# Kernel optimization log

Hardware: AMD Instinct MI355X
Metric: run time of the kernel (lower is better)

The kernel has to match this reference:

```python
import jax, jax.numpy as jnp
import numpy as np

EPS = 1e-5

def _conv1x1(x, w):
    # w: [out_ch, in_ch], x: [n, c, h, w] -> [n, out_ch, h, w]
    return jnp.einsum('oc,nchw->nohw', w, x)

def _bn_relu(x, g, b, m, v):
    # inference-mode BatchNorm2d followed by ReLU
    s = g * jax.lax.rsqrt(v + EPS)
    return jax.nn.relu(x * s[None, :, None, None] + (b - m * s)[None, :, None, None])

def setup_inputs() -> dict:
    N, C, H, W, Kc, K = 8, 512, 128, 128, 512, 19
    keys = iter(jax.random.split(jax.random.key(0), 64))
    d = {}
    d['x'] = jax.random.normal(next(keys), (N, C, H, W), jnp.float32)
    d['proxy'] = jax.random.normal(next(keys), (N, C, K, 1), jnp.float32)
    for nm, shp in [('wp1', (Kc, C)), ('wp2', (Kc, Kc)), ('wo1', (Kc, C)),
                    ('wo2', (Kc, Kc)), ('wd', (Kc, C)), ('wu', (C, Kc))]:
        d[nm] = jax.random.normal(next(keys), shp, jnp.float32) * np.float32(1.0 / np.sqrt(shp[1]))
    for tag, ch in [('p1', Kc), ('p2', Kc), ('o1', Kc), ('o2', Kc), ('d', Kc), ('u', C)]:
        d['g' + tag] = 1.0 + 0.1 * jax.random.normal(next(keys), (ch,), jnp.float32)
        d['b' + tag] = 0.1 * jax.random.normal(next(keys), (ch,), jnp.float32)
        d['m' + tag] = 0.1 * jax.random.normal(next(keys), (ch,), jnp.float32)
        d['v' + tag] = jax.random.uniform(next(keys), (ch,), jnp.float32, 0.5, 1.5)
    return d

def reference(x, proxy,
              wp1, gp1, bp1, mp1, vp1, wp2, gp2, bp2, mp2, vp2,
              wo1, go1, bo1, mo1, vo1, wo2, go2, bo2, mo2, vo2,
              wd, gd, bd, md, vd, wu, gu, bu, mu, vu):
    # scale == 1: no pooling / upsampling
    # f_pixel: two 1x1 conv + BN + ReLU on pixel features
    q = _bn_relu(_conv1x1(x, wp1), gp1, bp1, mp1, vp1)
    q = _bn_relu(_conv1x1(q, wp2), gp2, bp2, mp2, vp2)        # [n, kc, h, w]
    n, kc, h, w = q.shape
    q = q.reshape(n, kc, h * w)                               # [n, kc, hw]
    # f_object on proxy (object region representations)
    k = _bn_relu(_conv1x1(proxy, wo1), go1, bo1, mo1, vo1)
    k = _bn_relu(_conv1x1(k, wo2), go2, bo2, mo2, vo2).reshape(n, kc, -1)  # [n, kc, K]
    # f_down (value)
    v = _bn_relu(_conv1x1(proxy, wd), gd, bd, md, vd).reshape(n, kc, -1)   # [n, kc, K]
    # cross-attention: pixels attend over object regions
    sim = jnp.einsum('ncq,nck->nqk', q, k) * (kc ** -0.5)     # [n, hw, K]
    attn = jax.nn.softmax(sim, axis=-1)
    ctx = jnp.einsum('nqk,nck->ncq', attn, v).reshape(n, kc, h, w)
    # f_up: 1x1 conv + BN + ReLU back to in_channels
    return _bn_relu(_conv1x1(ctx, wu), gu, bu, mu, vu)
```

## Files before the change

### kernel.cpp

```cpp
#include <hip/hip_runtime.h>
#include <stdint.h>

#define HW 16384
#define CH 512
#define KR 19

typedef float f32x4 __attribute__((ext_vector_type(4)));
typedef _Float16 half8 __attribute__((ext_vector_type(8)));
typedef unsigned short us8 __attribute__((ext_vector_type(8)));
typedef unsigned short us4 __attribute__((ext_vector_type(4)));

__device__ __forceinline__ unsigned short f2h(float f) {
    union { _Float16 h; unsigned short u; } v; v.h = (_Float16)f; return v.u;
}
__device__ __forceinline__ float h2f(unsigned short u) {
    union { unsigned short u; _Float16 h; } v; v.u = u; return (float)v.h;
}

__device__ __forceinline__ void gll16(const void* g, void* l) {
    __builtin_amdgcn_global_load_lds(
        (const __attribute__((address_space(1))) unsigned int*)g,
        (__attribute__((address_space(3))) unsigned int*)l,
        16, 0, 0);
}

__global__ void ObjectAttentionBlock_1176821039805_kernel() {}

__global__ __launch_bounds__(256) void prep_kernel(
    const float* __restrict__ wp1, const float* __restrict__ wp2, const float* __restrict__ wu,
    unsigned short* __restrict__ wp1h, unsigned short* __restrict__ wp2h, unsigned short* __restrict__ wuh,
    const float* gp1, const float* bp1, const float* mp1, const float* vp1,
    const float* gp2, const float* bp2, const float* mp2, const float* vp2,
    const float* gu,  const float* bu,  const float* mu,  const float* vu,
    float* __restrict__ cons)
{
    int i = blockIdx.x * 256 + threadIdx.x;
    if (i < CH * CH) {
        wp1h[i] = f2h(wp1[i]);
        wp2h[i] = f2h(wp2[i]);
        wuh[i]  = f2h(wu[i]);
    }
    if (i < CH) {
        float s1 = gp1[i] * rsqrtf(vp1[i] + 1e-5f);
        cons[i] = s1;          cons[512 + i]  = bp1[i] - mp1[i] * s1;
        float s2 = gp2[i] * rsqrtf(vp2[i] + 1e-5f);
        cons[1024 + i] = s2;   cons[1536 + i] = bp2[i] - mp2[i] * s2;
        float su = gu[i] * rsqrtf(vu[i] + 1e-5f);
        cons[2048 + i] = su;   cons[2560 + i] = bu[i] - mu[i] * su;
    }
}

__global__ __launch_bounds__(256) void transpose_kernel(
    const float* __restrict__ x, unsigned short* __restrict__ xT)
{
    __shared__ unsigned short t[64][66];
    const int n  = blockIdx.z;
    const int c0 = blockIdx.y * 64;
    const int m0 = blockIdx.x * 64;
    const int tx = threadIdx.x & 63;
    const int ty = threadIdx.x >> 6;
    const float* xb = x + ((size_t)n * CH + c0) * HW + m0;
    #pragma unroll
    for (int r = 0; r < 16; ++r) {
        int cl = ty * 16 + r;
        t[cl][tx] = f2h(xb[(size_t)cl * HW + tx]);
    }
    __syncthreads();
    unsigned short* xo = xT + ((size_t)n * HW + m0) * CH + c0;
    #pragma unroll
    for (int r = 0; r < 16; ++r) {
        int ml = ty * 16 + r;
        xo[(size_t)ml * CH + tx] = t[tx][ml];
    }
}

__global__ __launch_bounds__(256) void kv1_kernel(
    const float* __restrict__ proxy, const float* __restrict__ wo1, const float* __restrict__ wd,
    const float* go1, const float* bo1, const float* mo1, const float* vo1,
    const float* gd,  const float* bd,  const float* md,  const float* vd,
    float* __restrict__ t1, float* __restrict__ vout)
{
    const int n  = blockIdx.x;
    const int o0 = blockIdx.y * 64;
    const float* px = proxy + (size_t)n * CH * KR;
    for (int idx = threadIdx.x; idx < 64 * KR; idx += 256) {
        int o = o0 + idx / KR;
        int j = idx % KR;
        float a1 = 0.f, a2 = 0.f;
        for (int c = 0; c < CH; ++c) {
            float p = px[c * KR + j];
            a1 += wo1[o * CH + c] * p;
            a2 += wd [o * CH + c] * p;
        }
        float s1 = go1[o] * rsqrtf(vo1[o] + 1e-5f);
        float s2 = gd[o]  * rsqrtf(vd[o]  + 1e-5f);
        t1  [((size_t)n * CH + o) * KR + j] = fmaxf(a1 * s1 + (bo1[o] - mo1[o] * s1), 0.f);
        vout[((size_t)n * CH + o) * KR + j] = fmaxf(a2 * s2 + (bd[o]  - md[o]  * s2), 0.f);
    }
}

__global__ __launch_bounds__(256) void kv2_kernel(
    const float* __restrict__ t1, const float* __restrict__ wo2,
    const float* go2, const float* bo2, const float* mo2, const float* vo2,
    float* __restrict__ kout)
{
    const int n  = blockIdx.x;
    const int o0 = blockIdx.y * 64;
    const float* tb = t1 + (size_t)n * CH * KR;
    for (int idx = threadIdx.x; idx < 64 * KR; idx += 256) {
        int o = o0 + idx / KR;
        int j = idx % KR;
        float a = 0.f;
        for (int c = 0; c < CH; ++c) a += wo2[o * CH + c] * tb[c * KR + j];
        float s = go2[o] * rsqrtf(vo2[o] + 1e-5f);
        kout[((size_t)n * CH + o) * KR + j] = fmaxf(a * s + (bo2[o] - mo2[o] * s), 0.f);
    }
}

__global__ __launch_bounds__(256) void pad_kernel(
    const float* __restrict__ kbuf, const float* __restrict__ vbuf,
    unsigned short* __restrict__ kt, unsigned short* __restrict__ vt)
{
    int idx = blockIdx.x * 256 + threadIdx.x;
    int n = idx >> 16, rem = idx & 65535;
    int j = rem >> 9, c = rem & 511;
    kt[idx] = (j < KR) ? f2h(kbuf[((size_t)(n * CH + c)) * KR + j]) : (unsigned short)0;
    int c2 = rem >> 7, j2 = rem & 127;
    vt[idx] = (j2 < KR) ? f2h(vbuf[((size_t)(n * CH + c2)) * KR + j2]) : (unsigned short)0;
}

template<int MODE, int BN>
__global__ __launch_bounds__(256) void gemm_nt(
    const unsigned short* __restrict__ A,
    const unsigned short* __restrict__ W,
    const float* __restrict__ sc, const float* __restrict__ sh,
    void* __restrict__ outp)
{
    __shared__ __align__(16) char lds_raw[33792];
    float (*epi)[132] = (float (*)[132])lds_raw;

    const int tid  = threadIdx.x;
    const int lane = tid & 63;
    const int wave = tid >> 6;
    const int wm = (tid >> 7) & 1;
    const int wn = (tid >> 6) & 1;
    const int id  = blockIdx.x;
    const int swz = (id & 7) * 512 + (id >> 3);
    const int i0 = (swz >> 2) << 7;
    const int j0 = (swz & 3) << 7;

    const int sl = lane >> 3;
    const int ss = lane & 7;
    const int sc_ = ss ^ sl;
    const int srow = sl + 64 * (sc_ >> 2);
    const int skof = (sc_ & 3) * 8;

    float scv[4], shv[4];
    #pragma unroll
    for (int j = 0; j < 4; ++j) {
        int gj = j0 + wn * 64 + j * 16 + (lane & 15);
        scv[j] = BN ? sc[gj] : 1.0f;
        shv[j] = BN ? sh[gj] : 0.0f;
    }
    asm volatile("s_waitcnt vmcnt(0)" ::: "memory");
    __builtin_amdgcn_sched_barrier(0);

    f32x4 acc[4][4];
    #pragma unroll
    for (int i = 0; i < 4; ++i)
        #pragma unroll
        for (int j = 0; j < 4; ++j) acc[i][j] = (f32x4){0.f, 0.f, 0.f, 0.f};

    const int rl  = lane & 15;
    const int kch = lane >> 4;

    auto stage = [&](int t) {
        char* db = lds_raw + (t & 1) * 16384;
        #pragma unroll
        for (int q = 0; q < 2; ++q) {
            int g = q * 4 + wave;
            gll16((const char*)A + ((size_t)(i0 + g * 8 + srow) * 512 + t * 32 + skof) * 2,
                  db + g * 1024);
            gll16((const char*)W + ((size_t)(j0 + g * 8 + srow) * 512 + t * 32 + skof) * 2,
                  db + 8192 + g * 1024);
        }
    };

    stage(0);
    stage(1);

    for (int t = 0; t < 16; ++t) {
        if (t < 15) asm volatile("s_waitcnt vmcnt(4)" ::: "memory");
        else        asm volatile("s_waitcnt vmcnt(0)" ::: "memory");
        __builtin_amdgcn_sched_barrier(0);
        __builtin_amdgcn_s_barrier();
        __builtin_amdgcn_sched_barrier(0);

        const unsigned short* st = (const unsigned short*)(lds_raw + (t & 1) * 16384);
        __builtin_amdgcn_s_setprio(1);
        half8 af[4], bw[4];
        #pragma unroll
        for (int u = 0; u < 4; ++u) {
            int la = rl + u * 16;
            af[u] = *(const half8*)(st + la * 64 + (((wm * 4 + kch) ^ (la & 7)) << 3));
            bw[u] = *(const half8*)(st + 4096 + la * 64 + (((wn * 4 + kch) ^ (la & 7)) << 3));
        }
        #pragma unroll
        for (int i = 0; i < 4; ++i)
            #pragma unroll
            for (int j = 0; j < 4; ++j)
                acc[i][j] = __builtin_amdgcn_mfma_f32_16x16x32_f16(af[i], bw[j], acc[i][j], 0, 0, 0);
        __builtin_amdgcn_s_setprio(0);
        __builtin_amdgcn_sched_barrier(0);
        __builtin_amdgcn_s_barrier();
        __builtin_amdgcn_sched_barrier(0);
        if (t < 14) stage(t + 2);
    }

    if (MODE == 0) {
        unsigned short* op = (unsigned short*)outp;
        #pragma unroll
        for (int i = 0; i < 4; ++i) {
            int gi = i0 + wm * 64 + i * 16 + (lane >> 4) * 4;
            #pragma unroll
            for (int j = 0; j < 4; ++j) {
                int gj = j0 + wn * 64 + j * 16 + (lane & 15);
                #pragma unroll
                for (int r = 0; r < 4; ++r) {
                    float vv = acc[i][j][r];
                    if (BN) vv = fmaxf(vv * scv[j] + shv[j], 0.f);
                    op[(size_t)(gi + r) * 512 + gj] = f2h(vv);
                }
            }
        }
    } else {
        float* op = (float*)outp;
        const int n  = i0 >> 14;
        const int mb = i0 & (HW - 1);
        #pragma unroll
        for (int h = 0; h < 2; ++h) {
            __syncthreads();
            if (wn == h) {
                #pragma unroll
                for (int j = 0; j < 4; ++j) {
                    int ljh = j * 16 + (lane & 15);
                    #pragma unroll
                    for (int i = 0; i < 4; ++i) {
                        int li = wm * 64 + i * 16 + (lane >> 4) * 4;
                        f32x4 vv;
                        #pragma unroll
                        for (int r = 0; r < 4; ++r)
                            vv[r] = fmaxf(acc[i][j][r] * scv[j] + shv[j], 0.f);
                        *(f32x4*)&epi[ljh][li] = vv;
                    }
                }
            }
            __syncthreads();
            #pragma unroll
            for (int q = 0; q < 8; ++q) {
                int idx = q * 256 + tid;
                int ch = idx >> 5, chunk = idx & 31;
                f32x4 v = *(const f32x4*)&epi[ch][chunk * 4];
                size_t base = ((size_t)(n * 512 + j0 + h * 64 + ch) << 14) + mb + chunk * 4;
                op[base] = v[0]; op[base + 1] = v[1]; op[base + 2] = v[2]; op[base + 3] = v[3];
            }
        }
    }
}

__global__ __launch_bounds__(256) void attn_fused(
    const unsigned short* __restrict__ q2,
    const unsigned short* __restrict__ ktg,
    const unsigned short* __restrict__ vtg,
    unsigned short* __restrict__ ctx)
{
    __shared__ __align__(16) char lds[47104];
    unsigned short* stage = (unsigned short*)lds;
    unsigned short* vt_l  = (unsigned short*)lds;
    unsigned short* att_l = (unsigned short*)(lds + 36864);

    const int tid  = threadIdx.x;
    const int lane = tid & 63;
    const int w    = tid >> 6;
    const int i0   = blockIdx.x * 128;
    const int n    = blockIdx.x >> 7;
    const unsigned short* KT = ktg + n * 65536;
    const unsigned short* VT = vtg + n * 65536;

    size_t gA[4]; int loA[4];
    #pragma unroll
    for (int q = 0; q < 4; ++q) {
        int ca = q * 256 + tid;
        int r = ca >> 3, p = ca & 7;
        gA[q] = (size_t)(i0 + r) * 512 + p * 8;
        loA[q] = r * 64 + ((p ^ (r & 7)) << 3);
    }
    const int rB = tid >> 3, pB = tid & 7;
    const size_t gB = (size_t)rB * 512 + pB * 8;
    const int loB = 8192 + rB * 64 + ((pB ^ (rB & 7)) << 3);

    us8 va[4], vbk;
    #pragma unroll
    for (int q = 0; q < 4; ++q) va[q] = *(const us8*)(q2 + gA[q]);
    vbk = *(const us8*)(KT + gB);

    f32x4 acc[2][2];
    #pragma unroll
    for (int i = 0; i < 2; ++i)
        #pragma unroll
        for (int j = 0; j < 2; ++j) acc[i][j] = (f32x4){0.f, 0.f, 0.f, 0.f};

    const int kch = lane >> 4;
    for (int kk = 0; kk < 8; ++kk) {
        __syncthreads();
        #pragma unroll
        for (int q = 0; q < 4; ++q) *(us8*)(stage + loA[q]) = va[q];
        *(us8*)(stage + loB) = vbk;
        __syncthreads();
        if (kk < 7) {
            #pragma unroll
            for (int q = 0; q < 4; ++q) va[q] = *(const us8*)(q2 + gA[q] + (kk + 1) * 64);
            vbk = *(const us8*)(KT + gB + (kk + 1) * 64);
        }
        #pragma unroll
        for (int s = 0; s < 2; ++s) {
            half8 af[2], bf[2];
            #pragma unroll
            for (int i = 0; i < 2; ++i) {
                int ra = w * 32 + i * 16 + (lane & 15);
                af[i] = *(const half8*)(stage + ra * 64 + (((s * 4 + kch) ^ (ra & 7)) << 3));
            }
            #pragma unroll
            for (int t = 0; t < 2; ++t) {
                int rb = t * 16 + (lane & 15);
                bf[t] = *(const half8*)(stage + 8192 + rb * 64 + (((s * 4 + kch) ^ (rb & 7)) << 3));
            }
            #pragma unroll
            for (int i = 0; i < 2; ++i)
                #pragma unroll
                for (int j = 0; j < 2; ++j)
                    acc[i][j] = __builtin_amdgcn_mfma_f32_16x16x32_f16(af[i], bf[j], acc[i][j], 0, 0, 0);
        }
    }

    const float scale = 0.044194173824159216f;
    const bool v1 = (lane & 15) < 3;
    unsigned short a16[2][4][2];
    #pragma unroll
    for (int i = 0; i < 2; ++i) {
        #pragma unroll
        for (int r = 0; r < 4; ++r) {
            float s0 = acc[i][0][r] * scale;
            float s1v = acc[i][1][r] * scale;
            float m = v1 ? fmaxf(s0, s1v) : s0;
            m = fmaxf(m, __shfl_xor(m, 1));
            m = fmaxf(m, __shfl_xor(m, 2));
            m = fmaxf(m, __shfl_xor(m, 4));
            m = fmaxf(m, __shfl_xor(m, 8));
            float a0 = __expf(s0 - m);
            float a1 = v1 ? __expf(s1v - m) : 0.f;
            float sm = a0 + a1;
            sm += __shfl_xor(sm, 1);
            sm += __shfl_xor(sm, 2);
            sm += __shfl_xor(sm, 4);
            sm += __shfl_xor(sm, 8);
            float inv = 1.0f / sm;
            a16[i][r][0] = f2h(a0 * inv);
            a16[i][r][1] = f2h(a1 * inv);
        }
    }
    #pragma unroll
    for (int i = 0; i < 2; ++i)
        #pragma unroll
        for (int r = 0; r < 4; ++r) {
            int R = w * 32 + i * 16 + (lane >> 4) * 4 + r;
            att_l[R * 40 + (lane & 15)]      = a16[i][r][0];
            att_l[R * 40 + 16 + (lane & 15)] = a16[i][r][1];
        }
    __syncthreads();

    #pragma unroll
    for (int q = 0; q < 8; ++q) {
        int id = q * 256 + tid;
        int c = id >> 2, part = id & 3;
        us8 v = *(const us8*)(VT + (size_t)c * 128 + part * 8);
        *(us4*)(vt_l + c * 36 + part * 8)     = (us4){v[0], v[1], v[2], v[3]};
        *(us4*)(vt_l + c * 36 + part * 8 + 4) = (us4){v[4], v[5], v[6], v[7]};
    }
    __syncthreads();

    half8 a2[2];
    #pragma unroll
    for (int i = 0; i < 2; ++i) {
        int R = w * 32 + i * 16 + (lane & 15);
        a2[i] = *(const half8*)(att_l + R * 40 + (lane >> 4) * 8);
    }
    #pragma unroll
    for (int jc = 0; jc < 4; ++jc) {
        half8 bf[8];
        #pragma unroll
        for (int t = 0; t < 8; ++t) {
            int c = jc * 128 + t * 16 + (lane & 15);
            const unsigned short* pb = vt_l + c * 36 + (lane >> 4) * 8;
            us4 lo = *(const us4*)(pb);
            us4 hi = *(const us4*)(pb + 4);
            us8 u = {lo[0], lo[1], lo[2], lo[3], hi[0], hi[1], hi[2], hi[3]};
            bf[t] = *(half8*)&u;
        }
        #pragma unroll
        for (int i = 0; i < 2; ++i) {
            #pragma unroll
            for (int t = 0; t < 8; ++t) {
                f32x4 o = __builtin_amdgcn_mfma_f32_16x16x32_f16(
                    a2[i], bf[t], (f32x4){0.f, 0.f, 0.f, 0.f}, 0, 0, 0);
                int col = jc * 128 + t * 16 + (lane & 15);
                int row = i0 + w * 32 + i * 16 + (lane >> 4) * 4;
                #pragma unroll
                for (int r = 0; r < 4; ++r)
                    ctx[(size_t)(row + r) * 512 + col] = f2h(o[r]);
            }
        }
    }
}

extern "C" void kernel_launch(void* const* d_in, const int* in_sizes, int n_in,
                              void* d_out, int out_size, void* d_ws, size_t ws_size,
                              hipStream_t stream)
{
    const float* x     = (const float*)d_in[0];
    const float* proxy = (const float*)d_in[1];
    const float* wp1   = (const float*)d_in[2];
    const float* wp2   = (const float*)d_in[3];
    const float* wo1   = (const float*)d_in[4];
    const float* wo2   = (const float*)d_in[5];
    const float* wd    = (const float*)d_in[6];
    const float* wu    = (const float*)d_in[7];
    const float* gp1 = (const float*)d_in[8],  *bp1 = (const float*)d_in[9];
    const float* mp1 = (const float*)d_in[10], *vp1 = (const float*)d_in[11];
    const float* gp2 = (const float*)d_in[12], *bp2 = (const float*)d_in[13];
    const float* mp2 = (const float*)d_in[14], *vp2 = (const float*)d_in[15];
    const float* go1 = (const float*)d_in[16], *bo1 = (const float*)d_in[17];
    const float* mo1 = (const float*)d_in[18], *vo1 = (const float*)d_in[19];
    const float* go2 = (const float*)d_in[20], *bo2 = (const float*)d_in[21];
    const float* mo2 = (const float*)d_in[22], *vo2 = (const float*)d_in[23];
    const float* gd  = (const float*)d_in[24], *bd  = (const float*)d_in[25];
    const float* md  = (const float*)d_in[26], *vd  = (const float*)d_in[27];
    const float* gu  = (const float*)d_in[28], *bu  = (const float*)d_in[29];
    const float* mu  = (const float*)d_in[30], *vu  = (const float*)d_in[31];

    char* ws = (char*)d_ws;
    unsigned short* r0   = (unsigned short*)ws;
    unsigned short* wp1h = (unsigned short*)(ws + 134217728);
    unsigned short* wp2h = wp1h + 262144;
    unsigned short* wuh  = wp2h + 262144;
    float* t1   = (float*)(wuh + 262144);
    float* kbuf = t1 + 8 * CH * KR;
    float* vbuf = kbuf + 8 * CH * KR;
    float* cons = vbuf + 8 * CH * KR;

    float* outf = (float*)d_out;
    unsigned short* outh = (unsigned short*)d_out;
    unsigned short* q1T = outh;
    unsigned short* ktb = outh + 117440512;
    unsigned short* vtb = outh + 117964800;

    prep_kernel<<<1024, 256, 0, stream>>>(wp1, wp2, wu, wp1h, wp2h, wuh,
        gp1, bp1, mp1, vp1, gp2, bp2, mp2, vp2, gu, bu, mu, vu, cons);
    transpose_kernel<<<dim3(256, 8, 8), 256, 0, stream>>>(x, r0);
    kv1_kernel<<<dim3(8, 8), 256, 0, stream>>>(proxy, wo1, wd,
        go1, bo1, mo1, vo1, gd, bd, md, vd, t1, vbuf);
    kv2_kernel<<<dim3(8, 8), 256, 0, stream>>>(t1, wo2, go2, bo2, mo2, vo2, kbuf);
    pad_kernel<<<2048, 256, 0, stream>>>(kbuf, vbuf, ktb, vtb);

    gemm_nt<0, 1><<<4096, 256, 0, stream>>>(r0, wp1h, cons, cons + 512, q1T);
    gemm_nt<0, 1><<<4096, 256, 0, stream>>>(q1T, wp2h, cons + 1024, cons + 1536, r0);
    attn_fused<<<1024, 256, 0, stream>>>(r0, ktb, vtb, r0);
    gemm_nt<1, 1><<<4096, 256, 0, stream>>>(r0, wuh, cons + 2048, cons + 2560, outf);
}
```

Before: 730.5 us.

## Triple-buffer GEMM LDS stages and drop second per-iteration barrier

The GEMM mainloop moves from double to triple buffering in LDS, 48KB instead of 33KB. The prefetch of tile t+2 is now issued right after the top barrier rather than after a second barrier at the end of the iteration, so one of the two workgroup barriers per k-step goes away. The template kernel is split into three named wrapper kernels around a shared device body. The larger LDS footprint may reduce how many workgroups fit per CU.

```diff
diff --git a/kernel.cpp b/kernel.cpp
--- a/kernel.cpp
+++ b/kernel.cpp
@@ -130,13 +130,12 @@
 }
 
 template<int MODE, int BN>
-__global__ __launch_bounds__(256) void gemm_nt(
+__device__ __forceinline__ void gemm_body(
     const unsigned short* __restrict__ A,
     const unsigned short* __restrict__ W,
     const float* __restrict__ sc, const float* __restrict__ sh,
-    void* __restrict__ outp)
-{
-    __shared__ __align__(16) char lds_raw[33792];
+    void* __restrict__ outp, char* lds_raw)
+{
     float (*epi)[132] = (float (*)[132])lds_raw;
 
     const int tid  = threadIdx.x;
@@ -175,7 +174,7 @@
     const int kch = lane >> 4;
 
     auto stage = [&](int t) {
-        char* db = lds_raw + (t & 1) * 16384;
+        char* db = lds_raw + (t % 3) * 16384;
         #pragma unroll
         for (int q = 0; q < 2; ++q) {
             int g = q * 4 + wave;
@@ -195,8 +194,10 @@
         __builtin_amdgcn_sched_barrier(0);
         __builtin_amdgcn_s_barrier();
         __builtin_amdgcn_sched_barrier(0);
-
-        const unsigned short* st = (const unsigned short*)(lds_raw + (t & 1) * 16384);
+        if (t < 14) stage(t + 2);
+        __builtin_amdgcn_sched_barrier(0);
+
+        const unsigned short* st = (const unsigned short*)(lds_raw + (t % 3) * 16384);
         __builtin_amdgcn_s_setprio(1);
         half8 af[4], bw[4];
         #pragma unroll
@@ -212,9 +213,6 @@
                 acc[i][j] = __builtin_amdgcn_mfma_f32_16x16x32_f16(af[i], bw[j], acc[i][j], 0, 0, 0);
         __builtin_amdgcn_s_setprio(0);
         __builtin_amdgcn_sched_barrier(0);
-        __builtin_amdgcn_s_barrier();
-        __builtin_amdgcn_sched_barrier(0);
-        if (t < 14) stage(t + 2);
     }
 
     if (MODE == 0) {
@@ -266,6 +264,28 @@
             }
         }
     }
+}
+
+__global__ __launch_bounds__(256) void gemm_q1(
+    const unsigned short* __restrict__ A, const unsigned short* __restrict__ W,
+    const float* __restrict__ sc, const float* __restrict__ sh, void* __restrict__ outp)
+{
+    __shared__ __align__(16) char lds[49152];
+    gemm_body<0, 1>(A, W, sc, sh, outp, lds);
+}
+__global__ __launch_bounds__(256) void gemm_q2(
+    const unsigned short* __restrict__ A, const unsigned short* __restrict__ W,
+    const float* __restrict__ sc, const float* __restrict__ sh, void* __restrict__ outp)
+{
+    __shared__ __align__(16) char lds[49152];
+    gemm_body<0, 1>(A, W, sc, sh, outp, lds);
+}
+__global__ __launch_bounds__(256) void gemm_out(
+    const unsigned short* __restrict__ A, const unsigned short* __restrict__ W,
+    const float* __restrict__ sc, const float* __restrict__ sh, void* __restrict__ outp)
+{
+    __shared__ __align__(16) char lds[49152];
+    gemm_body<1, 1>(A, W, sc, sh, outp, lds);
 }
 
 __global__ __launch_bounds__(256) void attn_fused(
@@ -472,8 +492,8 @@
     kv2_kernel<<<dim3(8, 8), 256, 0, stream>>>(t1, wo2, go2, bo2, mo2, vo2, kbuf);
     pad_kernel<<<2048, 256, 0, stream>>>(kbuf, vbuf, ktb, vtb);
 
-    gemm_nt<0, 1><<<4096, 256, 0, stream>>>(r0, wp1h, cons, cons + 512, q1T);
-    gemm_nt<0, 1><<<4096, 256, 0, stream>>>(q1T, wp2h, cons + 1024, cons + 1536, r0);
+    gemm_q1<<<4096, 256, 0, stream>>>(r0, wp1h, cons, cons + 512, q1T);
+    gemm_q2<<<4096, 256, 0, stream>>>(q1T, wp2h, cons + 1024, cons + 1536, r0);
     attn_fused<<<1024, 256, 0, stream>>>(r0, ktb, vtb, r0);
-    gemm_nt<1, 1><<<4096, 256, 0, stream>>>(r0, wuh, cons + 2048, cons + 2560, outf);
-}
+    gemm_out<<<4096, 256, 0, stream>>>(r0, wuh, cons + 2048, cons + 2560, outf);
+}
```

New measurement: 724.1 us. Within noise of the previous version (-0.9%).
